# Kernel tuning notes

Measured on AMD Instinct MI355X. Metric: run time of the kernel, lower is better.

Reference implementation:

```python
import jax, jax.numpy as jnp
import numpy as np

NEG_SLOPE = 0.2
EPS = 1e-16


def gat_layer(x, src, dst, Ws, Wd, a_s, a_d, b, heads, out_c, concat):
    # x: [N, F_in]; Ws/Wd: [F_in, heads*out_c]; a_s/a_d: [heads, out_c]; b: [heads*out_c] or [out_c]
    N = x.shape[0]
    xs = (x @ Ws).reshape(N, heads, out_c)  # src-projected features
    xd = (x @ Wd).reshape(N, heads, out_c)  # dst-projected features
    al_s = (xs * a_s).sum(-1)  # [N, H]
    al_d = (xd * a_d).sum(-1)  # [N, H]
    e = jax.nn.leaky_relu(al_s[src] + al_d[dst], negative_slope=NEG_SLOPE)  # [E, H]
    m = jax.ops.segment_max(e, dst, num_segments=N)  # [N, H], -inf for isolated nodes
    m = jnp.where(jnp.isfinite(m), m, 0.0)
    ex = jnp.exp(e - m[dst])
    den = jax.ops.segment_sum(ex, dst, num_segments=N)  # [N, H]
    alpha = ex / (den[dst] + EPS)  # segment softmax over incoming edges
    msg = xs[src] * alpha[:, :, None]  # [E, H, C]
    out = jax.ops.segment_sum(msg, dst, num_segments=N)  # [N, H, C]
    out = out.reshape(N, heads * out_c) if concat else out.mean(axis=1)
    return out + b


def setup_inputs() -> dict:
    key = jax.random.key(0)
    ks = jax.random.split(key, 20)
    N, E, F_in, H, Ch, Co = 50000, 400000, 128, 4, 128, 16
    s = lambda k, shp, fan: jax.random.normal(k, shp, dtype=jnp.float32) * (1.0 / np.sqrt(fan))
    inp = {
        "x": jax.random.normal(ks[0], (N, F_in), dtype=jnp.float32),
        "edge_index": jax.random.randint(ks[1], (2, E), 0, N, dtype=jnp.int32),
        # layer 1: in=128 -> heads=4, C=128, concat
        "Ws1": s(ks[2], (F_in, H * Ch), F_in), "Wd1": s(ks[3], (F_in, H * Ch), F_in),
        "as1": s(ks[4], (H, Ch), Ch), "ad1": s(ks[5], (H, Ch), Ch),
        "b1": jnp.zeros((H * Ch,), dtype=jnp.float32),
        # layer 2: in=512 -> heads=4, C=128, concat
        "Ws2": s(ks[6], (H * Ch, H * Ch), H * Ch), "Wd2": s(ks[7], (H * Ch, H * Ch), H * Ch),
        "as2": s(ks[8], (H, Ch), Ch), "ad2": s(ks[9], (H, Ch), Ch),
        "b2": jnp.zeros((H * Ch,), dtype=jnp.float32),
        # layer 3: in=512 -> heads=1, C=16, no concat
        "Ws3": s(ks[10], (H * Ch, Co), H * Ch), "Wd3": s(ks[11], (H * Ch, Co), H * Ch),
        "as3": s(ks[12], (1, Co), Co), "ad3": s(ks[13], (1, Co), Co),
        "b3": jnp.zeros((Co,), dtype=jnp.float32),
    }
    return inp


def reference(x, edge_index, Ws1, Wd1, as1, ad1, b1, Ws2, Wd2, as2, ad2, b2, Ws3, Wd3, as3, ad3, b3):
    src, dst = edge_index[0], edge_index[1]
    h = gat_layer(x, src, dst, Ws1, Wd1, as1, ad1, b1, heads=4, out_c=128, concat=True)
    h = jax.nn.relu(h)  # dropout = identity in eval mode
    h = gat_layer(h, src, dst, Ws2, Wd2, as2, ad2, b2, heads=4, out_c=128, concat=True)
    h = jax.nn.relu(h)
    out = gat_layer(h, src, dst, Ws3, Wd3, as3, ad3, b3, heads=1, out_c=16, concat=False)
    return out
```

## Files before the change

### kernel.cpp

```cpp
#include <hip/hip_runtime.h>
#include <math.h>

#define NEG_SLOPE 0.2f
#define EPSF 1e-16f

typedef _Float16 h2v __attribute__((ext_vector_type(2)));
typedef _Float16 h4v __attribute__((ext_vector_type(4)));
typedef _Float16 h8v __attribute__((ext_vector_type(8)));
typedef float f4v __attribute__((ext_vector_type(4)));

#define AS1 __attribute__((address_space(1)))
#define AS3 __attribute__((address_space(3)))

__device__ __forceinline__ void gll16(const void* g, void* l) {
  __builtin_amdgcn_global_load_lds((AS1 void*)g, (AS3 void*)l, 16, 0, 0);
}


__global__ void hist_kernel(const int* __restrict__ dst, int* __restrict__ counts, int E) {
  int t = blockIdx.x * 256 + threadIdx.x;
  if (t < E) atomicAdd(&counts[dst[t]], 1);
}

__global__ void scan1(const int* __restrict__ counts, int* __restrict__ offs,
                      int* __restrict__ bsum, int N) {
  __shared__ int sd[1024];
  int tid = threadIdx.x;
  int i = blockIdx.x * 1024 + tid;
  int v = (i < N) ? counts[i] : 0;
  sd[tid] = v;
  __syncthreads();
  for (int s = 1; s < 1024; s <<= 1) {
    int tv = (tid >= s) ? sd[tid - s] : 0;
    __syncthreads();
    sd[tid] += tv;
    __syncthreads();
  }
  if (i < N) offs[i] = sd[tid] - v;
  if (tid == 1023) bsum[blockIdx.x] = sd[1023];
}

__global__ void scan2(int* __restrict__ bsum, int* __restrict__ offs, int nb, int N, int E) {
  if (threadIdx.x == 0) {
    int r = 0;
    for (int i = 0; i < nb; i++) { int v = bsum[i]; bsum[i] = r; r += v; }
    offs[N] = E;
  }
}

__global__ void scan3(int* __restrict__ offs, const int* __restrict__ bsum, int N) {
  int i = blockIdx.x * 1024 + threadIdx.x;
  if (i < N) offs[i] += bsum[blockIdx.x];
}

__global__ void scatter_kernel(const int* __restrict__ src, const int* __restrict__ dst,
                               const int* __restrict__ off, int* __restrict__ cur,
                               int* __restrict__ srcp, int E) {
  int t = blockIdx.x * 256 + threadIdx.x;
  if (t < E) {
    int d = dst[t];
    int p = off[d] + atomicAdd(&cur[d], 1);
    srcp[p] = src[t];
  }
}


__global__ void convX(const float* __restrict__ x, _Float16* __restrict__ xh, int n4) {
  int i = blockIdx.x * 256 + threadIdx.x;
  if (i >= n4) return;
  float4 v = ((const float4*)x)[i];
  h4v h;
  h[0] = (_Float16)v.x; h[1] = (_Float16)v.y;
  h[2] = (_Float16)v.z; h[3] = (_Float16)v.w;
  ((h4v*)xh)[i] = h;
}

__global__ void convW(const float* __restrict__ W, _Float16* __restrict__ Th, int K) {
  __shared__ float tile[32][33];
  int bx = blockIdx.x * 32;
  int by = blockIdx.y * 32;
  int tx = threadIdx.x, ty = threadIdx.y;
#pragma unroll
  for (int i = 0; i < 32; i += 8)
    tile[ty + i][tx] = W[(size_t)(by + ty + i) * 512 + bx + tx];
  __syncthreads();
#pragma unroll
  for (int i = 0; i < 32; i += 8)
    Th[(size_t)(bx + ty + i) * K + by + tx] = (_Float16)tile[tx][ty + i];
}

__global__ void convW3(const float* __restrict__ W, _Float16* __restrict__ Th) {
  int t = blockIdx.x * 256 + threadIdx.x;
  if (t >= 512 * 16) return;
  int k = t >> 4, c = t & 15;
  Th[c * 512 + k] = (_Float16)W[t];
}


#define STAGE(bs, kt)                                  \
  do {                                                 \
    const size_t ko = (size_t)(kt) + w * 8;            \
    char* d0 = sm + (bs) + (w * 128) * 16;             \
    char* d1 = d0 + 1024;                              \
    gll16(A + (tm + l) * K + ko,      d0);             \
    gll16(A + (tm + 64 + l) * K + ko, d1);             \
    gll16(Bh + (cn + l) * K + ko,      d0 + 8192);     \
    gll16(Bh + (cn + 64 + l) * K + ko, d1 + 8192);     \
  } while (0)

template <int K>
__global__ __launch_bounds__(256) void gemm_f16(
    const _Float16* __restrict__ A, const _Float16* __restrict__ Bh,
    _Float16* __restrict__ C, int M) {
  __shared__ __align__(16) char sm[32768];
  const int t = threadIdx.x;
  const int w = t >> 6, l = t & 63;
  const int wr = w >> 1, wc = w & 1;
  const int kg = l >> 4, rr = l & 15;

  const int nwg = gridDim.x;
  const int q = nwg >> 3, r = nwg & 7;
  const int orig = blockIdx.x;
  const int xcd = orig & 7, slot = orig >> 3;
  const int wgid = (xcd < r ? xcd * (q + 1) : r * (q + 1) + (xcd - r) * q) + slot;
  const size_t tm = (size_t)(wgid >> 2) * 128;
  const size_t cn = (size_t)(wgid & 3) * 128;

  f4v acc[4][4];
#pragma unroll
  for (int i = 0; i < 4; i++)
#pragma unroll
    for (int j = 0; j < 4; j++) acc[i][j] = (f4v){0.f, 0.f, 0.f, 0.f};

  STAGE(0, 0);
  __syncthreads();
  int cur = 0;

  for (int kt = 0; kt < K; kt += 32) {
    if (kt + 32 < K) STAGE(cur ^ 16384, kt + 32);

    const char* base = sm + cur;
    h8v ah[4], bh[4];
#pragma unroll
    for (int i = 0; i < 4; i++) {
      int ca = (kg * 128 + wr * 64 + i * 16 + rr) * 16;
      int cb = (kg * 128 + wc * 64 + i * 16 + rr) * 16;
      ah[i] = *(const h8v*)(base + ca);
      bh[i] = *(const h8v*)(base + 8192 + cb);
    }
#pragma unroll
    for (int i = 0; i < 4; i++)
#pragma unroll
      for (int j = 0; j < 4; j++)
        acc[i][j] = __builtin_amdgcn_mfma_f32_16x16x32_f16(ah[i], bh[j], acc[i][j], 0, 0, 0);
    __syncthreads();
    cur ^= 16384;
  }

#pragma unroll
  for (int i = 0; i < 4; i++) {
    int row0 = wr * 64 + i * 16 + (l >> 4) * 4;
#pragma unroll
    for (int j = 0; j < 4; j++) {
      int col = wc * 64 + j * 16 + rr;
#pragma unroll
      for (int r2 = 0; r2 < 4; r2++) {
        size_t row = tm + row0 + r2;
        if (row < (size_t)M) C[row * 512 + cn + col] = (_Float16)acc[i][j][r2];
      }
    }
  }
}


__global__ __launch_bounds__(256) void gemm3(const _Float16* __restrict__ A,
                                             const _Float16* __restrict__ Bth,
                                             float* __restrict__ C, int M) {
  int wv = threadIdx.x >> 6, l = threadIdx.x & 63;
  size_t tm = ((size_t)blockIdx.x * 4 + wv) * 16;
  if (tm >= (size_t)M) return;
  int rr = l & 15, kg = l >> 4;
  f4v acc = (f4v){0.f, 0.f, 0.f, 0.f};
  for (int kt = 0; kt < 512; kt += 32) {
    int ka = kt + kg * 8;
    h8v a_h = *(const h8v*)&A[(tm + rr) * 512 + ka];
    h8v b_h = *(const h8v*)&Bth[rr * 512 + ka];
    acc = __builtin_amdgcn_mfma_f32_16x16x32_f16(a_h, b_h, acc, 0, 0, 0);
  }
#pragma unroll
  for (int r = 0; r < 4; r++) {
    size_t row = tm + kg * 4 + r;
    if (row < (size_t)M) C[row * 16 + rr] = acc[r];
  }
}


__global__ void wsd_kernel(const float* __restrict__ Wd, const float* __restrict__ a_d,
                           float* __restrict__ wsd, int K, int H, int C) {
  int g = (blockIdx.x * 256 + threadIdx.x) >> 4;
  int l16 = threadIdx.x & 15;
  if (g >= K * H) return;
  int k = g / H, h = g - k * H;
  int ce = C >> 4;
  float s = 0.f;
  for (int j = 0; j < ce; j++) {
    int c = l16 * ce + j;
    s += Wd[(size_t)k * (H * C) + h * C + c] * a_d[h * C + c];
  }
#pragma unroll
  for (int o = 1; o < 16; o <<= 1) s += __shfl_xor(s, o);
  if (l16 == 0) wsd[k * H + h] = s;
}


__global__ void al_f16(const _Float16* __restrict__ xs, const _Float16* __restrict__ ih,
                       const float* __restrict__ a_s, const float* __restrict__ wsd,
                       float* __restrict__ als, float* __restrict__ ald, int N, int K) {
  int wid = threadIdx.x >> 6, lane = threadIdx.x & 63;
  int n = blockIdx.x * 4 + wid;
  if (n >= N) return;
  h8v vx = *(const h8v*)&xs[(size_t)n * 512 + lane * 8];
  float s = 0.f;
#pragma unroll
  for (int j = 0; j < 8; j++) s += (float)vx[j] * a_s[lane * 8 + j];
  for (int o = 1; o < 16; o <<= 1) s += __shfl_xor(s, o);
  if (!(lane & 15)) als[n * 4 + (lane >> 4)] = s;

  float d0 = 0.f, d1 = 0.f, d2 = 0.f, d3 = 0.f;
  int k0 = lane * 8;
  if (k0 < K) {
    h8v qh = *(const h8v*)&ih[(size_t)n * K + k0];
#pragma unroll
    for (int j = 0; j < 8; j++) {
      float xv = (float)qh[j];
      float4 wv = *(const float4*)&wsd[(k0 + j) * 4];
      d0 += xv * wv.x; d1 += xv * wv.y; d2 += xv * wv.z; d3 += xv * wv.w;
    }
  }
  for (int o = 1; o < 64; o <<= 1) {
    d0 += __shfl_xor(d0, o); d1 += __shfl_xor(d1, o);
    d2 += __shfl_xor(d2, o); d3 += __shfl_xor(d3, o);
  }
  if (lane == 0) *(float4*)&ald[n * 4] = make_float4(d0, d1, d2, d3);
}

__global__ void al3_f16(const float* __restrict__ xs3, const _Float16* __restrict__ ih,
                        const float* __restrict__ as3, const float* __restrict__ wsd,
                        float* __restrict__ als, float* __restrict__ ald, int N) {
  int wid = threadIdx.x >> 6, lane = threadIdx.x & 63;
  int n = blockIdx.x * 4 + wid;
  if (n >= N) return;
  float s = (lane < 16) ? xs3[(size_t)n * 16 + lane] * as3[lane] : 0.f;
  for (int o = 1; o < 16; o <<= 1) s += __shfl_xor(s, o);
  h8v qh = *(const h8v*)&ih[(size_t)n * 512 + lane * 8];
  float d = 0.f;
#pragma unroll
  for (int j = 0; j < 8; j++) d += (float)qh[j] * wsd[lane * 8 + j];
  for (int o = 1; o < 64; o <<= 1) d += __shfl_xor(d, o);
  if (lane == 0) { als[n] = s; ald[n] = d; }
}


__global__ void wgt4_kernel(const float* __restrict__ als, const float* __restrict__ ald,
                            const int* __restrict__ off, const int* __restrict__ srcp,
                            _Float16* __restrict__ wgt, int N) {
  int wid = threadIdx.x >> 6, lane = threadIdx.x & 63;
  int n = blockIdx.x * 4 + wid;
  if (n >= N) return;
  int h = lane & 3, e = lane >> 2;
  float aldn = ald[n * 4 + h];
  int p0 = off[n], deg = off[n + 1] - p0;
  if (deg == 0) return;
  float ev0 = -1e30f;
  if (e < deg) {
    float v = als[srcp[p0 + e] * 4 + h] + aldn;
    ev0 = (v > 0.f) ? v : NEG_SLOPE * v;
  }
  float m = ev0;
  for (int base = 16; base < deg; base += 16) {
    float ev = -1e30f;
    if (base + e < deg) {
      float v = als[srcp[p0 + base + e] * 4 + h] + aldn;
      ev = (v > 0.f) ? v : NEG_SLOPE * v;
    }
    m = fmaxf(m, ev);
  }
#pragma unroll
  for (int o = 4; o < 64; o <<= 1) m = fmaxf(m, __shfl_xor(m, o));
  float den = (e < deg) ? __expf(ev0 - m) : 0.f;
  for (int base = 16; base < deg; base += 16) {
    if (base + e < deg) {
      float v = als[srcp[p0 + base + e] * 4 + h] + aldn;
      v = (v > 0.f) ? v : NEG_SLOPE * v;
      den += __expf(v - m);
    }
  }
#pragma unroll
  for (int o = 4; o < 64; o <<= 1) den += __shfl_xor(den, o);
  float rw = 1.f / (den + EPSF);
  if (e < deg) wgt[(size_t)(p0 + e) * 4 + h] = (_Float16)(__expf(ev0 - m) * rw);
  for (int base = 16; base < deg; base += 16) {
    if (base + e < deg) {
      float v = als[srcp[p0 + base + e] * 4 + h] + aldn;
      v = (v > 0.f) ? v : NEG_SLOPE * v;
      wgt[(size_t)(p0 + base + e) * 4 + h] = (_Float16)(__expf(v - m) * rw);
    }
  }
}

__global__ void wgt1_kernel(const float* __restrict__ als, const float* __restrict__ ald,
                            const int* __restrict__ off, const int* __restrict__ srcp,
                            _Float16* __restrict__ wgt, int N) {
  int wid = threadIdx.x >> 6, lane = threadIdx.x & 63;
  int n = blockIdx.x * 4 + wid;
  if (n >= N) return;
  float aldn = ald[n];
  int p0 = off[n], deg = off[n + 1] - p0;
  if (deg == 0) return;
  float ev0 = -1e30f;
  if (lane < deg) {
    float v = als[srcp[p0 + lane]] + aldn;
    ev0 = (v > 0.f) ? v : NEG_SLOPE * v;
  }
  float m = ev0;
  for (int base = 64; base < deg; base += 64) {
    float ev = -1e30f;
    if (base + lane < deg) {
      float v = als[srcp[p0 + base + lane]] + aldn;
      ev = (v > 0.f) ? v : NEG_SLOPE * v;
    }
    m = fmaxf(m, ev);
  }
#pragma unroll
  for (int o = 1; o < 64; o <<= 1) m = fmaxf(m, __shfl_xor(m, o));
  float den = (lane < deg) ? __expf(ev0 - m) : 0.f;
  for (int base = 64; base < deg; base += 64) {
    if (base + lane < deg) {
      float v = als[srcp[p0 + base + lane]] + aldn;
      v = (v > 0.f) ? v : NEG_SLOPE * v;
      den += __expf(v - m);
    }
  }
#pragma unroll
  for (int o = 1; o < 64; o <<= 1) den += __shfl_xor(den, o);
  float rw = 1.f / (den + EPSF);
  if (lane < deg) wgt[p0 + lane] = (_Float16)(__expf(ev0 - m) * rw);
  for (int base = 64; base < deg; base += 64) {
    if (base + lane < deg) {
      float v = als[srcp[p0 + base + lane]] + aldn;
      v = (v > 0.f) ? v : NEG_SLOPE * v;
      wgt[p0 + base + lane] = (_Float16)(__expf(v - m) * rw);
    }
  }
}


__global__ __launch_bounds__(256) void agg512(
    const _Float16* __restrict__ xs, const _Float16* __restrict__ wgt,
    const int* __restrict__ off, const int* __restrict__ srcp,
    const float* __restrict__ bias, _Float16* __restrict__ oh, int N) {
  int n = blockIdx.x;
  int t = threadIdx.x;
  int h = t >> 6;
  int p0 = off[n], p1 = off[n + 1];
  float ax = 0.f, ay = 0.f, bx = 0.f, by = 0.f;
  int p = p0;
  for (; p + 1 < p1; p += 2) {
    int s0 = srcp[p], s1 = srcp[p + 1];
    float w0 = (float)wgt[(size_t)p * 4 + h];
    float w1 = (float)wgt[(size_t)(p + 1) * 4 + h];
    h2v v0 = *(const h2v*)&xs[(size_t)s0 * 512 + 2 * t];
    h2v v1 = *(const h2v*)&xs[(size_t)s1 * 512 + 2 * t];
    ax += w0 * (float)v0[0]; ay += w0 * (float)v0[1];
    bx += w1 * (float)v1[0]; by += w1 * (float)v1[1];
  }
  if (p < p1) {
    int s0 = srcp[p];
    float w0 = (float)wgt[(size_t)p * 4 + h];
    h2v v0 = *(const h2v*)&xs[(size_t)s0 * 512 + 2 * t];
    ax += w0 * (float)v0[0]; ay += w0 * (float)v0[1];
  }
  ax += bx; ay += by;
  float2 b = *(const float2*)&bias[2 * t];
  ax = fmaxf(ax + b.x, 0.f);
  ay = fmaxf(ay + b.y, 0.f);
  h2v wh;
  wh[0] = (_Float16)ax; wh[1] = (_Float16)ay;
  *(h2v*)&oh[(size_t)n * 512 + 2 * t] = wh;
}

__global__ void agg16(const float* __restrict__ xs3, const _Float16* __restrict__ wgt,
                      const int* __restrict__ off, const int* __restrict__ srcp,
                      const float* __restrict__ bias, float* __restrict__ out, int N) {
  int g = threadIdx.x >> 4, c = threadIdx.x & 15;
  int n = blockIdx.x * 16 + g;
  if (n >= N) return;
  int p0 = off[n], p1 = off[n + 1];
  float acc = 0.f;
  for (int p = p0; p < p1; p++)
    acc += (float)wgt[p] * xs3[(size_t)srcp[p] * 16 + c];
  out[(size_t)n * 16 + c] = acc + bias[c];
}


extern "C" void kernel_launch(void* const* d_in, const int* in_sizes, int n_in,
                              void* d_out, int out_size, void* d_ws, size_t ws_size,
                              hipStream_t stream) {
  const float* x   = (const float*)d_in[0];
  const int*   ei  = (const int*)d_in[1];
  const float* Ws1 = (const float*)d_in[2];
  const float* Wd1 = (const float*)d_in[3];
  const float* as1 = (const float*)d_in[4];
  const float* ad1 = (const float*)d_in[5];
  const float* b1  = (const float*)d_in[6];
  const float* Ws2 = (const float*)d_in[7];
  const float* Wd2 = (const float*)d_in[8];
  const float* as2 = (const float*)d_in[9];
  const float* ad2 = (const float*)d_in[10];
  const float* b2  = (const float*)d_in[11];
  const float* Ws3 = (const float*)d_in[12];
  const float* Wd3 = (const float*)d_in[13];
  const float* as3 = (const float*)d_in[14];
  const float* ad3 = (const float*)d_in[15];
  const float* b3  = (const float*)d_in[16];

  const int N = in_sizes[0] / 128;
  const int E = in_sizes[1] / 2;
  const int* src = ei;
  const int* dst = ei + E;

  char* w = (char*)d_ws;
  _Float16* xs     = (_Float16*)(w + 0);
  _Float16* hbuf   = (_Float16*)(w + 51200000);
  float*    als    = (float*)(w + 102400000);
  float*    ald    = (float*)(w + 103200000);
  float*    xs3    = (float*)(w + 104000000);
  _Float16* wgt    = (_Float16*)(w + 107200000);
  int*      counts = (int*)(w + 110400000);
  int*      cur    = (int*)(w + 110600000);
  int*      offs   = (int*)(w + 110800000);
  int*      bsum   = (int*)(w + 111000192);
  int*      srcp   = (int*)(w + 111004288);
  float*    wsd    = (float*)(w + 112604288);
  _Float16* wt_hi  = (_Float16*)(w + 112612480);
  _Float16* wt3_hi = (_Float16*)(w + 113136768);

  hipMemsetAsync(counts, 0, 2 * (size_t)N * 4, stream);
  hist_kernel<<<(E + 255) / 256, 256, 0, stream>>>(dst, counts, E);
  int nb = (N + 1023) / 1024;
  scan1<<<nb, 1024, 0, stream>>>(counts, offs, bsum, N);
  scan2<<<1, 64, 0, stream>>>(bsum, offs, nb, N, E);
  scan3<<<nb, 1024, 0, stream>>>(offs, bsum, N);
  scatter_kernel<<<(E + 255) / 256, 256, 0, stream>>>(src, dst, offs, cur, srcp, E);

  int ggrid = ((N + 127) / 128) * 4;
  dim3 cwb(32, 8);
  int nwb = (N + 3) / 4;

  convX<<<(N * 128 / 4 + 255) / 256, 256, 0, stream>>>(x, hbuf, N * 128 / 4);
  wsd_kernel<<<(128 * 4 * 16 + 255) / 256, 256, 0, stream>>>(Wd1, ad1, wsd, 128, 4, 128);
  convW<<<dim3(16, 4), cwb, 0, stream>>>(Ws1, wt_hi, 128);
  gemm_f16<128><<<ggrid, 256, 0, stream>>>(hbuf, wt_hi, xs, N);
  al_f16<<<nwb, 256, 0, stream>>>(xs, hbuf, as1, wsd, als, ald, N, 128);
  wgt4_kernel<<<nwb, 256, 0, stream>>>(als, ald, offs, srcp, wgt, N);
  agg512<<<N, 256, 0, stream>>>(xs, wgt, offs, srcp, b1, hbuf, N);

  wsd_kernel<<<(512 * 4 * 16 + 255) / 256, 256, 0, stream>>>(Wd2, ad2, wsd, 512, 4, 128);
  convW<<<dim3(16, 16), cwb, 0, stream>>>(Ws2, wt_hi, 512);
  gemm_f16<512><<<ggrid, 256, 0, stream>>>(hbuf, wt_hi, xs, N);
  al_f16<<<nwb, 256, 0, stream>>>(xs, hbuf, as2, wsd, als, ald, N, 512);
  wgt4_kernel<<<nwb, 256, 0, stream>>>(als, ald, offs, srcp, wgt, N);
  agg512<<<N, 256, 0, stream>>>(xs, wgt, offs, srcp, b2, hbuf, N);

  wsd_kernel<<<(512 * 16 + 255) / 256, 256, 0, stream>>>(Wd3, ad3, wsd, 512, 1, 16);
  convW3<<<32, 256, 0, stream>>>(Ws3, wt3_hi);
  gemm3<<<(N / 16 + 4) / 4, 256, 0, stream>>>(hbuf, wt3_hi, xs3, N);
  al3_f16<<<nwb, 256, 0, stream>>>(xs3, hbuf, as3, wsd, als, ald, N);
  wgt1_kernel<<<nwb, 256, 0, stream>>>(als, ald, offs, srcp, wgt, N);
  agg16<<<(N + 15) / 16, 256, 0, stream>>>(xs3, wgt, offs, srcp, b3, (float*)d_out, N);
}
```

Baseline: 577.9 us.

## Fuse attention-logit computation into GEMM epilogue and edge-weight kernels

Computes the source attention logits (al_s) inside the GEMM epilogue, reducing per-row dot products across lanes and both column-waves through shared memory. The destination logits are now computed inside the edge-weight kernels, so the separate al_f16/al3_f16 kernels and the ald buffer go away. The 512-wide aggregation kernel switches to 128 threads with 4-wide half loads. This cuts a full read of xs and a kernel launch per layer, in exchange for extra shuffles and register pressure in the GEMM epilogue and a per-node dot product in the weight kernels.

```diff
diff --git a/kernel.cpp b/kernel.cpp
--- a/kernel.cpp
+++ b/kernel.cpp
@@ -111,7 +111,8 @@
 template <int K>
 __global__ __launch_bounds__(256) void gemm_f16(
     const _Float16* __restrict__ A, const _Float16* __restrict__ Bh,
-    _Float16* __restrict__ C, int M) {
+    const float* __restrict__ a_s, _Float16* __restrict__ C,
+    float* __restrict__ als, int M) {
   __shared__ __align__(16) char sm[32768];
   const int t = threadIdx.x;
   const int w = t >> 6, l = t & 63;
@@ -157,17 +158,43 @@
     cur ^= 16384;
   }
 
+  float sp[16];
+#pragma unroll
+  for (int k = 0; k < 16; k++) sp[k] = 0.f;
 #pragma unroll
   for (int i = 0; i < 4; i++) {
-    int row0 = wr * 64 + i * 16 + (l >> 4) * 4;
+    int row0 = wr * 64 + i * 16 + kg * 4;
 #pragma unroll
     for (int j = 0; j < 4; j++) {
       int col = wc * 64 + j * 16 + rr;
+      float aw = a_s[cn + col];
 #pragma unroll
       for (int r2 = 0; r2 < 4; r2++) {
+        float v = acc[i][j][r2];
         size_t row = tm + row0 + r2;
-        if (row < (size_t)M) C[row * 512 + cn + col] = (_Float16)acc[i][j][r2];
+        if (row < (size_t)M) C[row * 512 + cn + col] = (_Float16)v;
+        sp[i * 4 + r2] += v * aw;
       }
+    }
+  }
+#pragma unroll
+  for (int o = 1; o < 16; o <<= 1)
+#pragma unroll
+    for (int k = 0; k < 16; k++) sp[k] += __shfl_xor(sp[k], o);
+  float* ap = (float*)sm;
+  if (wc == 0 && rr == 0) {
+#pragma unroll
+    for (int k = 0; k < 16; k++)
+      ap[wr * 64 + (k >> 2) * 16 + kg * 4 + (k & 3)] = sp[k];
+  }
+  __syncthreads();
+  if (wc == 1 && rr == 0) {
+    int head = (int)(cn >> 7);
+#pragma unroll
+    for (int k = 0; k < 16; k++) {
+      int row = wr * 64 + (k >> 2) * 16 + kg * 4 + (k & 3);
+      size_t grow = tm + row;
+      if (grow < (size_t)M) als[grow * 4 + head] = ap[row] + sp[k];
     }
   }
 }
@@ -175,7 +202,9 @@
 
 __global__ __launch_bounds__(256) void gemm3(const _Float16* __restrict__ A,
                                              const _Float16* __restrict__ Bth,
-                                             float* __restrict__ C, int M) {
+                                             const float* __restrict__ as3,
+                                             float* __restrict__ C,
+                                             float* __restrict__ als, int M) {
   int wv = threadIdx.x >> 6, l = threadIdx.x & 63;
   size_t tm = ((size_t)blockIdx.x * 4 + wv) * 16;
   if (tm >= (size_t)M) return;
@@ -187,10 +216,21 @@
     h8v b_h = *(const h8v*)&Bth[rr * 512 + ka];
     acc = __builtin_amdgcn_mfma_f32_16x16x32_f16(a_h, b_h, acc, 0, 0, 0);
   }
+  float aw = as3[rr];
+  float s[4];
+#pragma unroll
+  for (int r = 0; r < 4; r++) s[r] = acc[r] * aw;
+#pragma unroll
+  for (int o = 1; o < 16; o <<= 1)
+#pragma unroll
+    for (int r = 0; r < 4; r++) s[r] += __shfl_xor(s[r], o);
 #pragma unroll
   for (int r = 0; r < 4; r++) {
     size_t row = tm + kg * 4 + r;
-    if (row < (size_t)M) C[row * 16 + rr] = acc[r];
+    if (row < (size_t)M) {
+      C[row * 16 + rr] = acc[r];
+      if (rr == 0) als[row] = s[r];
+    }
   }
 }
 
@@ -213,64 +253,46 @@
 }
 
 
-__global__ void al_f16(const _Float16* __restrict__ xs, const _Float16* __restrict__ ih,
-                       const float* __restrict__ a_s, const float* __restrict__ wsd,
-                       float* __restrict__ als, float* __restrict__ ald, int N, int K) {
+template <int K>
+__global__ void wgt4_kernel(const float* __restrict__ als, const _Float16* __restrict__ hin,
+                            const float* __restrict__ wsd, const int* __restrict__ off,
+                            const int* __restrict__ srcp, _Float16* __restrict__ wgt, int N) {
   int wid = threadIdx.x >> 6, lane = threadIdx.x & 63;
   int n = blockIdx.x * 4 + wid;
   if (n >= N) return;
-  h8v vx = *(const h8v*)&xs[(size_t)n * 512 + lane * 8];
-  float s = 0.f;
-#pragma unroll
-  for (int j = 0; j < 8; j++) s += (float)vx[j] * a_s[lane * 8 + j];
-  for (int o = 1; o < 16; o <<= 1) s += __shfl_xor(s, o);
-  if (!(lane & 15)) als[n * 4 + (lane >> 4)] = s;
-
-  float d0 = 0.f, d1 = 0.f, d2 = 0.f, d3 = 0.f;
-  int k0 = lane * 8;
-  if (k0 < K) {
-    h8v qh = *(const h8v*)&ih[(size_t)n * K + k0];
-#pragma unroll
-    for (int j = 0; j < 8; j++) {
-      float xv = (float)qh[j];
-      float4 wv = *(const float4*)&wsd[(k0 + j) * 4];
-      d0 += xv * wv.x; d1 += xv * wv.y; d2 += xv * wv.z; d3 += xv * wv.w;
-    }
-  }
-  for (int o = 1; o < 64; o <<= 1) {
-    d0 += __shfl_xor(d0, o); d1 += __shfl_xor(d1, o);
-    d2 += __shfl_xor(d2, o); d3 += __shfl_xor(d3, o);
-  }
-  if (lane == 0) *(float4*)&ald[n * 4] = make_float4(d0, d1, d2, d3);
-}
-
-__global__ void al3_f16(const float* __restrict__ xs3, const _Float16* __restrict__ ih,
-                        const float* __restrict__ as3, const float* __restrict__ wsd,
-                        float* __restrict__ als, float* __restrict__ ald, int N) {
-  int wid = threadIdx.x >> 6, lane = threadIdx.x & 63;
-  int n = blockIdx.x * 4 + wid;
-  if (n >= N) return;
-  float s = (lane < 16) ? xs3[(size_t)n * 16 + lane] * as3[lane] : 0.f;
-  for (int o = 1; o < 16; o <<= 1) s += __shfl_xor(s, o);
-  h8v qh = *(const h8v*)&ih[(size_t)n * 512 + lane * 8];
-  float d = 0.f;
-#pragma unroll
-  for (int j = 0; j < 8; j++) d += (float)qh[j] * wsd[lane * 8 + j];
-  for (int o = 1; o < 64; o <<= 1) d += __shfl_xor(d, o);
-  if (lane == 0) { als[n] = s; ald[n] = d; }
-}
-
-
-__global__ void wgt4_kernel(const float* __restrict__ als, const float* __restrict__ ald,
-                            const int* __restrict__ off, const int* __restrict__ srcp,
-                            _Float16* __restrict__ wgt, int N) {
-  int wid = threadIdx.x >> 6, lane = threadIdx.x & 63;
-  int n = blockIdx.x * 4 + wid;
-  if (n >= N) return;
-  int h = lane & 3, e = lane >> 2;
-  float aldn = ald[n * 4 + h];
   int p0 = off[n], deg = off[n + 1] - p0;
   if (deg == 0) return;
+
+  float d0 = 0.f, d1 = 0.f, d2 = 0.f, d3 = 0.f;
+  constexpr int KP = K / 64;
+  {
+    int k0 = lane * KP;
+    if constexpr (K == 512) {
+      h8v qv = *(const h8v*)&hin[(size_t)n * K + k0];
+#pragma unroll
+      for (int j = 0; j < 8; j++) {
+        float xv = (float)qv[j];
+        float4 wv = *(const float4*)&wsd[(k0 + j) * 4];
+        d0 += xv * wv.x; d1 += xv * wv.y; d2 += xv * wv.z; d3 += xv * wv.w;
+      }
+    } else {
+      h2v qv = *(const h2v*)&hin[(size_t)n * K + k0];
+#pragma unroll
+      for (int j = 0; j < KP; j++) {
+        float xv = (float)qv[j];
+        float4 wv = *(const float4*)&wsd[(k0 + j) * 4];
+        d0 += xv * wv.x; d1 += xv * wv.y; d2 += xv * wv.z; d3 += xv * wv.w;
+      }
+    }
+#pragma unroll
+    for (int o = 1; o < 64; o <<= 1) {
+      d0 += __shfl_xor(d0, o); d1 += __shfl_xor(d1, o);
+      d2 += __shfl_xor(d2, o); d3 += __shfl_xor(d3, o);
+    }
+  }
+  int h = lane & 3, e = lane >> 2;
+  float aldn = (h == 0) ? d0 : (h == 1) ? d1 : (h == 2) ? d2 : d3;
+
   float ev0 = -1e30f;
   if (e < deg) {
     float v = als[srcp[p0 + e] * 4 + h] + aldn;
@@ -308,15 +330,24 @@
   }
 }
 
-__global__ void wgt1_kernel(const float* __restrict__ als, const float* __restrict__ ald,
-                            const int* __restrict__ off, const int* __restrict__ srcp,
-                            _Float16* __restrict__ wgt, int N) {
+__global__ void wgt1_kernel(const float* __restrict__ als, const _Float16* __restrict__ hin,
+                            const float* __restrict__ wsd, const int* __restrict__ off,
+                            const int* __restrict__ srcp, _Float16* __restrict__ wgt, int N) {
   int wid = threadIdx.x >> 6, lane = threadIdx.x & 63;
   int n = blockIdx.x * 4 + wid;
   if (n >= N) return;
-  float aldn = ald[n];
   int p0 = off[n], deg = off[n + 1] - p0;
   if (deg == 0) return;
+
+  float aldn = 0.f;
+  {
+    h8v qv = *(const h8v*)&hin[(size_t)n * 512 + lane * 8];
+#pragma unroll
+    for (int j = 0; j < 8; j++) aldn += (float)qv[j] * wsd[lane * 8 + j];
+#pragma unroll
+    for (int o = 1; o < 64; o <<= 1) aldn += __shfl_xor(aldn, o);
+  }
+
   float ev0 = -1e30f;
   if (lane < deg) {
     float v = als[srcp[p0 + lane]] + aldn;
@@ -355,38 +386,43 @@
 }
 
 
-__global__ __launch_bounds__(256) void agg512(
+__global__ __launch_bounds__(128) void agg512(
     const _Float16* __restrict__ xs, const _Float16* __restrict__ wgt,
     const int* __restrict__ off, const int* __restrict__ srcp,
     const float* __restrict__ bias, _Float16* __restrict__ oh, int N) {
   int n = blockIdx.x;
   int t = threadIdx.x;
-  int h = t >> 6;
+  int h = t >> 5;
   int p0 = off[n], p1 = off[n + 1];
-  float ax = 0.f, ay = 0.f, bx = 0.f, by = 0.f;
+  float a0 = 0.f, a1 = 0.f, a2 = 0.f, a3 = 0.f;
+  float c0 = 0.f, c1 = 0.f, c2 = 0.f, c3 = 0.f;
   int p = p0;
   for (; p + 1 < p1; p += 2) {
     int s0 = srcp[p], s1 = srcp[p + 1];
     float w0 = (float)wgt[(size_t)p * 4 + h];
     float w1 = (float)wgt[(size_t)(p + 1) * 4 + h];
-    h2v v0 = *(const h2v*)&xs[(size_t)s0 * 512 + 2 * t];
-    h2v v1 = *(const h2v*)&xs[(size_t)s1 * 512 + 2 * t];
-    ax += w0 * (float)v0[0]; ay += w0 * (float)v0[1];
-    bx += w1 * (float)v1[0]; by += w1 * (float)v1[1];
+    h4v v0 = *(const h4v*)&xs[(size_t)s0 * 512 + 4 * t];
+    h4v v1 = *(const h4v*)&xs[(size_t)s1 * 512 + 4 * t];
+    a0 += w0 * (float)v0[0]; a1 += w0 * (float)v0[1];
+    a2 += w0 * (float)v0[2]; a3 += w0 * (float)v0[3];
+    c0 += w1 * (float)v1[0]; c1 += w1 * (float)v1[1];
+    c2 += w1 * (float)v1[2]; c3 += w1 * (float)v1[3];
   }
   if (p < p1) {
     int s0 = srcp[p];
     float w0 = (float)wgt[(size_t)p * 4 + h];
-    h2v v0 = *(const h2v*)&xs[(size_t)s0 * 512 + 2 * t];
-    ax += w0 * (float)v0[0]; ay += w0 * (float)v0[1];
-  }
-  ax += bx; ay += by;
-  float2 b = *(const float2*)&bias[2 * t];
-  ax = fmaxf(ax + b.x, 0.f);
-  ay = fmaxf(ay + b.y, 0.f);
-  h2v wh;
-  wh[0] = (_Float16)ax; wh[1] = (_Float16)ay;
-  *(h2v*)&oh[(size_t)n * 512 + 2 * t] = wh;
+    h4v v0 = *(const h4v*)&xs[(size_t)s0 * 512 + 4 * t];
+    a0 += w0 * (float)v0[0]; a1 += w0 * (float)v0[1];
+    a2 += w0 * (float)v0[2]; a3 += w0 * (float)v0[3];
+  }
+  a0 += c0; a1 += c1; a2 += c2; a3 += c3;
+  float4 b = *(const float4*)&bias[4 * t];
+  a0 = fmaxf(a0 + b.x, 0.f); a1 = fmaxf(a1 + b.y, 0.f);
+  a2 = fmaxf(a2 + b.z, 0.f); a3 = fmaxf(a3 + b.w, 0.f);
+  h4v wh;
+  wh[0] = (_Float16)a0; wh[1] = (_Float16)a1;
+  wh[2] = (_Float16)a2; wh[3] = (_Float16)a3;
+  *(h4v*)&oh[(size_t)n * 512 + 4 * t] = wh;
 }
 
 __global__ void agg16(const float* __restrict__ xs3, const _Float16* __restrict__ wgt,
@@ -433,7 +469,6 @@
   _Float16* xs     = (_Float16*)(w + 0);
   _Float16* hbuf   = (_Float16*)(w + 51200000);
   float*    als    = (float*)(w + 102400000);
-  float*    ald    = (float*)(w + 103200000);
   float*    xs3    = (float*)(w + 104000000);
   _Float16* wgt    = (_Float16*)(w + 107200000);
   int*      counts = (int*)(w + 110400000);
@@ -460,22 +495,19 @@
   convX<<<(N * 128 / 4 + 255) / 256, 256, 0, stream>>>(x, hbuf, N * 128 / 4);
   wsd_kernel<<<(128 * 4 * 16 + 255) / 256, 256, 0, stream>>>(Wd1, ad1, wsd, 128, 4, 128);
   convW<<<dim3(16, 4), cwb, 0, stream>>>(Ws1, wt_hi, 128);
-  gemm_f16<128><<<ggrid, 256, 0, stream>>>(hbuf, wt_hi, xs, N);
-  al_f16<<<nwb, 256, 0, stream>>>(xs, hbuf, as1, wsd, als, ald, N, 128);
-  wgt4_kernel<<<nwb, 256, 0, stream>>>(als, ald, offs, srcp, wgt, N);
-  agg512<<<N, 256, 0, stream>>>(xs, wgt, offs, srcp, b1, hbuf, N);
+  gemm_f16<128><<<ggrid, 256, 0, stream>>>(hbuf, wt_hi, as1, xs, als, N);
+  wgt4_kernel<128><<<nwb, 256, 0, stream>>>(als, hbuf, wsd, offs, srcp, wgt, N);
+  agg512<<<N, 128, 0, stream>>>(xs, wgt, offs, srcp, b1, hbuf, N);
 
   wsd_kernel<<<(512 * 4 * 16 + 255) / 256, 256, 0, stream>>>(Wd2, ad2, wsd, 512, 4, 128);
   convW<<<dim3(16, 16), cwb, 0, stream>>>(Ws2, wt_hi, 512);
-  gemm_f16<512><<<ggrid, 256, 0, stream>>>(hbuf, wt_hi, xs, N);
-  al_f16<<<nwb, 256, 0, stream>>>(xs, hbuf, as2, wsd, als, ald, N, 512);
-  wgt4_kernel<<<nwb, 256, 0, stream>>>(als, ald, offs, srcp, wgt, N);
-  agg512<<<N, 256, 0, stream>>>(xs, wgt, offs, srcp, b2, hbuf, N);
+  gemm_f16<512><<<ggrid, 256, 0, stream>>>(hbuf, wt_hi, as2, xs, als, N);
+  wgt4_kernel<512><<<nwb, 256, 0, stream>>>(als, hbuf, wsd, offs, srcp, wgt, N);
+  agg512<<<N, 128, 0, stream>>>(xs, wgt, offs, srcp, b2, hbuf, N);
 
   wsd_kernel<<<(512 * 16 + 255) / 256, 256, 0, stream>>>(Wd3, ad3, wsd, 512, 1, 16);
   convW3<<<32, 256, 0, stream>>>(Ws3, wt3_hi);
-  gemm3<<<(N / 16 + 4) / 4, 256, 0, stream>>>(hbuf, wt3_hi, xs3, N);
-  al3_f16<<<nwb, 256, 0, stream>>>(xs3, hbuf, as3, wsd, als, ald, N);
-  wgt1_kernel<<<nwb, 256, 0, stream>>>(als, ald, offs, srcp, wgt, N);
+  gemm3<<<(N / 16 + 4) / 4, 256, 0, stream>>>(hbuf, wt3_hi, as3, xs3, als, N);
+  wgt1_kernel<<<nwb, 256, 0, stream>>>(als, hbuf, wsd, offs, srcp, wgt, N);
   agg16<<<(N + 15) / 16, 256, 0, stream>>>(xs3, wgt, offs, srcp, b3, (float*)d_out, N);
 }
```

New measurement: 526.0 us. -9.0%, faster.
